# Optimization experiments

Measured on AMD Instinct MI355X. Metric: run time of the kernel, lower is better.

## Reference

```python
import jax, jax.numpy as jnp
import numpy as np

B, GX, GY = 4, 480, 360
C_IN, C_OUT = 64, 32
N = 480000

def setup_inputs() -> dict:
    key = jax.random.key(0)
    k1, k2, k3, k4, k5 = jax.random.split(key, 5)
    pt_fea = jax.random.normal(k1, (N, C_IN), dtype=jnp.float32)
    pt_ind = jax.random.randint(k2, (N, 2), 0, 360, dtype=jnp.int32)
    batch_idx = jax.random.randint(k3, (N,), 0, B, dtype=jnp.int32)
    W_comp = jax.random.normal(k4, (C_IN, C_OUT), dtype=jnp.float32) * 0.1
    b_comp = jax.random.normal(k5, (C_OUT,), dtype=jnp.float32) * 0.1
    return {"pt_fea": pt_fea, "pt_ind": pt_ind, "batch_idx": batch_idx,
            "W_comp": W_comp, "b_comp": b_comp}

def reference(pt_fea, pt_ind, batch_idx, W_comp, b_comp):
    # Linearized voxel key: (batch, x, y) -> flat segment id.
    # torch.unique + scatter_max over unique voxels followed by fancy-index
    # scatter into a zero grid is equivalent to a dense segment_max with
    # empty voxels forced to zero.
    seg = (batch_idx.astype(jnp.int32) * (GX * GY)
           + pt_ind[:, 0] * GY + pt_ind[:, 1])  # [N]
    num_seg = B * GX * GY
    pooled = jax.ops.segment_max(pt_fea, seg, num_segments=num_seg)  # [BV, C_IN]
    cnt = jax.ops.segment_sum(jnp.ones((pt_fea.shape[0],), jnp.float32), seg,
                              num_segments=num_seg)  # [BV]
    occupied = (cnt > 0)[:, None]
    pooled = jnp.where(occupied, pooled, 0.0)  # neutralize -inf of empty voxels
    # fea_compression: Linear + ReLU, applied to occupied voxels only
    comp = jax.nn.relu(pooled @ W_comp + b_comp)  # [BV, C_OUT]
    comp = jnp.where(occupied, comp, 0.0)
    out = comp.reshape(B, GX, GY, C_OUT)
    return jnp.transpose(out, (0, 3, 1, 2))  # [B, C_OUT, GX, GY]
```

## Files before the change

kernel.cpp:

```cpp
#include <hip/hip_runtime.h>

#define B_    4
#define GX_   480
#define GY_   360
#define GXGY  172800
#define NSEG  691200
#define CIN   64
#define COUT  32

__global__ __launch_bounds__(256) void build_lists_kernel(
    const int* __restrict__ ind,
    const int* __restrict__ bidx,
    int*       __restrict__ head,
    int*       __restrict__ next,
    int N)
{
    int i = blockIdx.x * 256 + threadIdx.x;
    if (i >= N) return;
    int2 xy = ((const int2*)ind)[i];
    int seg = bidx[i] * GXGY + xy.x * GY_ + xy.y;
    next[i] = atomicExch(&head[seg], i);
}

__global__ __launch_bounds__(256) void pool_compress_kernel(
    const float* __restrict__ fea,
    const int*   __restrict__ head,
    const int*   __restrict__ next,
    const float* __restrict__ W,
    const float* __restrict__ bias,
    float*       __restrict__ out)
{
    __shared__ float sW[CIN * COUT];
    __shared__ float sb[COUT];
    for (int j = threadIdx.x; j < CIN * COUT; j += 256) sW[j] = W[j];
    if (threadIdx.x < COUT) sb[threadIdx.x] = bias[threadIdx.x];
    __syncthreads();

    int v = blockIdx.x * 256 + threadIdx.x;
    int b = v / GXGY;
    int rem = v - b * GXGY;

    int i = head[v];
    float res[COUT];

    if (i >= 0) {
        float4 mx[CIN / 4];
        {
            const float4* fp = (const float4*)(fea + (size_t)i * CIN);
            #pragma unroll
            for (int q = 0; q < CIN / 4; ++q) mx[q] = fp[q];
            i = next[i];
        }
        while (i >= 0) {
            const float4* fp = (const float4*)(fea + (size_t)i * CIN);
            #pragma unroll
            for (int q = 0; q < CIN / 4; ++q) {
                float4 t = fp[q];
                mx[q].x = fmaxf(mx[q].x, t.x);
                mx[q].y = fmaxf(mx[q].y, t.y);
                mx[q].z = fmaxf(mx[q].z, t.z);
                mx[q].w = fmaxf(mx[q].w, t.w);
            }
            i = next[i];
        }

        float acc[COUT];
        #pragma unroll
        for (int c = 0; c < COUT; ++c) acc[c] = sb[c];
        #pragma unroll
        for (int q = 0; q < CIN / 4; ++q) {
            float f0 = mx[q].x, f1 = mx[q].y, f2 = mx[q].z, f3 = mx[q].w;
            const float* w0 = &sW[(q * 4 + 0) * COUT];
            const float* w1 = &sW[(q * 4 + 1) * COUT];
            const float* w2 = &sW[(q * 4 + 2) * COUT];
            const float* w3 = &sW[(q * 4 + 3) * COUT];
            #pragma unroll
            for (int c = 0; c < COUT; ++c) {
                acc[c] = fmaf(f0, w0[c], acc[c]);
                acc[c] = fmaf(f1, w1[c], acc[c]);
                acc[c] = fmaf(f2, w2[c], acc[c]);
                acc[c] = fmaf(f3, w3[c], acc[c]);
            }
        }
        #pragma unroll
        for (int c = 0; c < COUT; ++c) res[c] = fmaxf(acc[c], 0.0f);
    } else {
        #pragma unroll
        for (int c = 0; c < COUT; ++c) res[c] = 0.0f;
    }

    float* op = out + b * (COUT * GXGY) + rem;
    #pragma unroll
    for (int c = 0; c < COUT; ++c) op[c * GXGY] = res[c];
}

extern "C" void kernel_launch(void* const* d_in, const int* in_sizes, int n_in,
                              void* d_out, int out_size, void* d_ws, size_t ws_size,
                              hipStream_t stream)
{
    const float* fea  = (const float*)d_in[0];
    const int*   ind  = (const int*)d_in[1];
    const int*   bidx = (const int*)d_in[2];
    const float* W    = (const float*)d_in[3];
    const float* bias = (const float*)d_in[4];
    float*       out  = (float*)d_out;

    int N = in_sizes[0] / CIN;

    int* head = (int*)d_ws;
    int* next = (int*)d_ws + NSEG;

    hipMemsetAsync(head, 0xFF, (size_t)NSEG * sizeof(int), stream);

    build_lists_kernel<<<(N + 255) / 256, 256, 0, stream>>>(ind, bidx, head, next, N);
    pool_compress_kernel<<<NSEG / 256, 256, 0, stream>>>(fea, head, next, W, bias, out);
}
```

Before: 269.4 us.

## Pool voxels with wave-per-voxel coalesced reads and split channel compute across waves

The pooling kernel now has each 64-lane wavefront walk a voxel's point list, with every lane reading one feature channel, so each point row is fetched as one coalesced 256-byte access. Before, each thread walked its own voxel's list and loaded a full 64-float row with no reuse across the wave. The pooled rows go to padded shared memory. The linear layer is then split so each of the four waves computes 8 output channels for 64 voxels. This raises memory efficiency for the gather and lowers register pressure (no 64-float array per thread), at the cost of serialised list walks per wave and an extra block-wide sync.

```diff
diff --git a/kernel.cpp b/kernel.cpp
--- a/kernel.cpp
+++ b/kernel.cpp
@@ -1,12 +1,11 @@
 #include <hip/hip_runtime.h>
 
-#define B_    4
-#define GX_   480
-#define GY_   360
 #define GXGY  172800
 #define NSEG  691200
 #define CIN   64
 #define COUT  32
+#define VPB   64
+#define PSTR  (CIN + 1)
 
 __global__ __launch_bounds__(256) void build_lists_kernel(
     const int* __restrict__ ind,
@@ -18,7 +17,7 @@
     int i = blockIdx.x * 256 + threadIdx.x;
     if (i >= N) return;
     int2 xy = ((const int2*)ind)[i];
-    int seg = bidx[i] * GXGY + xy.x * GY_ + xy.y;
+    int seg = bidx[i] * GXGY + xy.x * 360 + xy.y;
     next[i] = atomicExch(&head[seg], i);
 }
 
@@ -32,66 +31,66 @@
 {
     __shared__ float sW[CIN * COUT];
     __shared__ float sb[COUT];
-    for (int j = threadIdx.x; j < CIN * COUT; j += 256) sW[j] = W[j];
-    if (threadIdx.x < COUT) sb[threadIdx.x] = bias[threadIdx.x];
+    __shared__ float sP[VPB * PSTR];
+    __shared__ int   sOcc[VPB];
+
+    int tid  = threadIdx.x;
+    int wid  = tid >> 6;
+    int lane = tid & 63;
+
+    for (int j = tid; j < CIN * COUT; j += 256) sW[j] = W[j];
+    if (tid < COUT) sb[tid] = bias[tid];
+
+    int vbase = blockIdx.x * VPB;
+
+    int myhead = (lane < 16) ? head[vbase + wid * 16 + lane] : -1;
+
+    for (int j = 0; j < 16; ++j) {
+        int lv = wid * 16 + j;
+        int i = __shfl(myhead, j);
+        if (i < 0) {
+            if (lane == 0) sOcc[lv] = 0;
+            continue;
+        }
+        if (lane == 0) sOcc[lv] = 1;
+        float m = fea[(size_t)i * CIN + lane];
+        i = next[i];
+        while (i >= 0) {
+            m = fmaxf(m, fea[(size_t)i * CIN + lane]);
+            i = next[i];
+        }
+        sP[lv * PSTR + lane] = m;
+    }
     __syncthreads();
 
-    int v = blockIdx.x * 256 + threadIdx.x;
-    int b = v / GXGY;
+    int lv = lane;
+    int g  = wid;
+    int v  = vbase + lv;
+    int b  = v / GXGY;
     int rem = v - b * GXGY;
 
-    int i = head[v];
-    float res[COUT];
-
-    if (i >= 0) {
-        float4 mx[CIN / 4];
-        {
-            const float4* fp = (const float4*)(fea + (size_t)i * CIN);
+    float res[8];
+    if (sOcc[lv]) {
+        float acc[8];
+        #pragma unroll
+        for (int c = 0; c < 8; ++c) acc[c] = sb[g * 8 + c];
+        #pragma unroll
+        for (int k = 0; k < CIN; ++k) {
+            float p = sP[lv * PSTR + k];
+            const float* w = &sW[k * COUT + g * 8];
             #pragma unroll
-            for (int q = 0; q < CIN / 4; ++q) mx[q] = fp[q];
-            i = next[i];
-        }
-        while (i >= 0) {
-            const float4* fp = (const float4*)(fea + (size_t)i * CIN);
-            #pragma unroll
-            for (int q = 0; q < CIN / 4; ++q) {
-                float4 t = fp[q];
-                mx[q].x = fmaxf(mx[q].x, t.x);
-                mx[q].y = fmaxf(mx[q].y, t.y);
-                mx[q].z = fmaxf(mx[q].z, t.z);
-                mx[q].w = fmaxf(mx[q].w, t.w);
-            }
-            i = next[i];
-        }
-
-        float acc[COUT];
-        #pragma unroll
-        for (int c = 0; c < COUT; ++c) acc[c] = sb[c];
-        #pragma unroll
-        for (int q = 0; q < CIN / 4; ++q) {
-            float f0 = mx[q].x, f1 = mx[q].y, f2 = mx[q].z, f3 = mx[q].w;
-            const float* w0 = &sW[(q * 4 + 0) * COUT];
-            const float* w1 = &sW[(q * 4 + 1) * COUT];
-            const float* w2 = &sW[(q * 4 + 2) * COUT];
-            const float* w3 = &sW[(q * 4 + 3) * COUT];
-            #pragma unroll
-            for (int c = 0; c < COUT; ++c) {
-                acc[c] = fmaf(f0, w0[c], acc[c]);
-                acc[c] = fmaf(f1, w1[c], acc[c]);
-                acc[c] = fmaf(f2, w2[c], acc[c]);
-                acc[c] = fmaf(f3, w3[c], acc[c]);
-            }
+            for (int c = 0; c < 8; ++c) acc[c] = fmaf(p, w[c], acc[c]);
         }
         #pragma unroll
-        for (int c = 0; c < COUT; ++c) res[c] = fmaxf(acc[c], 0.0f);
+        for (int c = 0; c < 8; ++c) res[c] = fmaxf(acc[c], 0.0f);
     } else {
         #pragma unroll
-        for (int c = 0; c < COUT; ++c) res[c] = 0.0f;
+        for (int c = 0; c < 8; ++c) res[c] = 0.0f;
     }
 
-    float* op = out + b * (COUT * GXGY) + rem;
+    float* op = out + (size_t)b * COUT * GXGY + (size_t)g * 8 * GXGY + rem;
     #pragma unroll
-    for (int c = 0; c < COUT; ++c) op[c * GXGY] = res[c];
+    for (int c = 0; c < 8; ++c) op[c * GXGY] = res[c];
 }
 
 extern "C" void kernel_launch(void* const* d_in, const int* in_sizes, int n_in,
@@ -111,7 +110,6 @@
     int* next = (int*)d_ws + NSEG;
 
     hipMemsetAsync(head, 0xFF, (size_t)NSEG * sizeof(int), stream);
-
     build_lists_kernel<<<(N + 255) / 256, 256, 0, stream>>>(ind, bidx, head, next, N);
-    pool_compress_kernel<<<NSEG / 256, 256, 0, stream>>>(fea, head, next, W, bias, out);
+    pool_compress_kernel<<<NSEG / VPB, 256, 0, stream>>>(fea, head, next, W, bias, out);
 }
```

After: 306.3 us. +13.7%, slower.
